# Performance work log

Hardware: AMD Instinct MI355X
Metric: run time of the kernel (lower is better)

The kernel has to match this reference:

```python
import jax, jax.numpy as jnp
import numpy as np
import math


def setup_inputs() -> dict:
    key = jax.random.key(0)
    n = 8192
    m = n * (n - 1) // 2  # 33550336
    compressed_matrix = jax.random.normal(key, (m,), dtype=jnp.float32)
    return {"compressed_matrix": compressed_matrix}


def reference(compressed_matrix) -> jnp.ndarray:
    m = compressed_matrix.shape[0]
    n = round(math.sqrt(2 * m)) + 1
    i, j = jnp.triu_indices(n, k=1)
    # scatter compressed vector into strict upper triangle
    upper = jnp.zeros((n, n), dtype=compressed_matrix.dtype).at[i, j].set(compressed_matrix)
    # symmetrize (diag of upper is zero, so subtracting diag is a no-op, kept for fidelity)
    sym = upper + upper.T - jnp.diag(jnp.diagonal(upper))
    return sym + jnp.eye(n, dtype=compressed_matrix.dtype)
```

## Files before the change

kernel.cpp:

```cpp
#include <hip/hip_runtime.h>
#include <math.h>

#define TILE 64

__global__ __launch_bounds__(256) void uncompress_sym_kernel(
    const float* __restrict__ comp, float* __restrict__ out, int n) {
    const int tr = blockIdx.y;
    const int tc = blockIdx.x;
    if (tc < tr) return;

    const int tid = threadIdx.x;
    __shared__ float s[TILE][TILE + 1];

    const int i0 = tr * TILE;
    const int j0 = tc * TILE;

    if (tr == tc) {
        for (int e = tid; e < TILE * TILE; e += 256) {
            const int y = e >> 6;
            const int x = e & 63;
            float v = 0.0f;
            if (x > y) {
                const int i = i0 + y;
                const int j = j0 + x;
                const int base = i * (2 * n - i - 1) / 2 - i - 1;
                v = comp[base + j];
            }
            s[y][x] = v;
        }
        __syncthreads();
        for (int e = tid; e < TILE * TILE; e += 256) {
            const int y = e >> 6;
            const int x = e & 63;
            float v;
            if (x > y)      v = s[y][x];
            else if (x == y) v = 1.0f;
            else            v = s[x][y];
            out[(size_t)(i0 + y) * n + (j0 + x)] = v;
        }
    } else {
        for (int it = 0; it < 4; ++it) {
            const int y  = (tid >> 4) + it * 16;
            const int x4 = (tid & 15) * 4;
            const int i  = i0 + y;
            const int base = i * (2 * n - i - 1) / 2 - i - 1;
            float4 v;
            __builtin_memcpy(&v, &comp[base + j0 + x4], sizeof(float4));
            *(float4*)&out[(size_t)i * n + (j0 + x4)] = v;
            s[y][x4 + 0] = v.x;
            s[y][x4 + 1] = v.y;
            s[y][x4 + 2] = v.z;
            s[y][x4 + 3] = v.w;
        }
        __syncthreads();
        for (int it = 0; it < 4; ++it) {
            const int y  = (tid >> 4) + it * 16;
            const int x4 = (tid & 15) * 4;
            float4 w;
            w.x = s[x4 + 0][y];
            w.y = s[x4 + 1][y];
            w.z = s[x4 + 2][y];
            w.w = s[x4 + 3][y];
            *(float4*)&out[(size_t)(j0 + y) * n + (i0 + x4)] = w;
        }
    }
}

extern "C" void kernel_launch(void* const* d_in, const int* in_sizes, int n_in,
                              void* d_out, int out_size, void* d_ws, size_t ws_size,
                              hipStream_t stream) {
    const float* comp = (const float*)d_in[0];
    float* out = (float*)d_out;
    const long long m = in_sizes[0];
    const int n = (int)llround(sqrt(2.0 * (double)m)) + 1;
    const int T = n / TILE;
    dim3 grid(T, T);
    uncompress_sym_kernel<<<grid, 256, 0, stream>>>(comp, out, n);
}
```

Before: 371.4 us.

## Launch only upper-triangle tiles, batch loads, use nontemporal stores

Replaces the full T×T grid, where half the blocks exit immediately, with a 1D grid over upper-triangle tiles only. Each block recovers its tile row and column from the linear block index with a sqrt estimate plus correction loops. All four row loads are issued before any store to expose more memory-level parallelism, and output writes use nontemporal stores so they do not pollute the cache. The cost is a few extra integer and float operations per block for the index mapping.

```diff
diff --git a/kernel.cpp b/kernel.cpp
--- a/kernel.cpp
+++ b/kernel.cpp
@@ -3,11 +3,16 @@
 
 #define TILE 64
 
+typedef float v4f  __attribute__((ext_vector_type(4)));
+typedef float v4fu __attribute__((ext_vector_type(4), aligned(4)));
+
 __global__ __launch_bounds__(256) void uncompress_sym_kernel(
-    const float* __restrict__ comp, float* __restrict__ out, int n) {
-    const int tr = blockIdx.y;
-    const int tc = blockIdx.x;
-    if (tc < tr) return;
+    const float* __restrict__ comp, float* __restrict__ out, int n, int T) {
+    const int b = blockIdx.x;
+    int tr = (int)((2 * T + 1 - sqrtf((float)((2 * T + 1) * (2 * T + 1) - 8 * b))) * 0.5f);
+    while (tr * T - tr * (tr - 1) / 2 > b) --tr;
+    while ((tr + 1) * T - (tr + 1) * tr / 2 <= b) ++tr;
+    const int tc = tr + (b - (tr * T - tr * (tr - 1) / 2));
 
     const int tid = threadIdx.x;
     __shared__ float s[TILE][TILE + 1];
@@ -15,16 +20,45 @@
     const int i0 = tr * TILE;
     const int j0 = tc * TILE;
 
-    if (tr == tc) {
+    if (tr != tc) {
+        const int x4 = (tid & 15) * 4;
+        const int yb = tid >> 4;
+        v4f v[4];
+#pragma unroll
+        for (int it = 0; it < 4; ++it) {
+            const int i = i0 + yb + it * 16;
+            const int base = i * (2 * n - i - 1) / 2 - i - 1;
+            v[it] = *(const v4fu*)&comp[base + j0 + x4];
+        }
+#pragma unroll
+        for (int it = 0; it < 4; ++it) {
+            const int y = yb + it * 16;
+            __builtin_nontemporal_store(v[it], (v4f*)&out[(size_t)(i0 + y) * n + (j0 + x4)]);
+            s[y][x4 + 0] = v[it].x;
+            s[y][x4 + 1] = v[it].y;
+            s[y][x4 + 2] = v[it].z;
+            s[y][x4 + 3] = v[it].w;
+        }
+        __syncthreads();
+#pragma unroll
+        for (int it = 0; it < 4; ++it) {
+            const int y = yb + it * 16;
+            v4f w;
+            w.x = s[x4 + 0][y];
+            w.y = s[x4 + 1][y];
+            w.z = s[x4 + 2][y];
+            w.w = s[x4 + 3][y];
+            __builtin_nontemporal_store(w, (v4f*)&out[(size_t)(j0 + y) * n + (i0 + x4)]);
+        }
+    } else {
         for (int e = tid; e < TILE * TILE; e += 256) {
             const int y = e >> 6;
             const int x = e & 63;
             float v = 0.0f;
             if (x > y) {
                 const int i = i0 + y;
-                const int j = j0 + x;
                 const int base = i * (2 * n - i - 1) / 2 - i - 1;
-                v = comp[base + j];
+                v = comp[base + j0 + x];
             }
             s[y][x] = v;
         }
@@ -33,35 +67,10 @@
             const int y = e >> 6;
             const int x = e & 63;
             float v;
-            if (x > y)      v = s[y][x];
+            if (x > y)       v = s[y][x];
             else if (x == y) v = 1.0f;
-            else            v = s[x][y];
-            out[(size_t)(i0 + y) * n + (j0 + x)] = v;
-        }
-    } else {
-        for (int it = 0; it < 4; ++it) {
-            const int y  = (tid >> 4) + it * 16;
-            const int x4 = (tid & 15) * 4;
-            const int i  = i0 + y;
-            const int base = i * (2 * n - i - 1) / 2 - i - 1;
-            float4 v;
-            __builtin_memcpy(&v, &comp[base + j0 + x4], sizeof(float4));
-            *(float4*)&out[(size_t)i * n + (j0 + x4)] = v;
-            s[y][x4 + 0] = v.x;
-            s[y][x4 + 1] = v.y;
-            s[y][x4 + 2] = v.z;
-            s[y][x4 + 3] = v.w;
-        }
-        __syncthreads();
-        for (int it = 0; it < 4; ++it) {
-            const int y  = (tid >> 4) + it * 16;
-            const int x4 = (tid & 15) * 4;
-            float4 w;
-            w.x = s[x4 + 0][y];
-            w.y = s[x4 + 1][y];
-            w.z = s[x4 + 2][y];
-            w.w = s[x4 + 3][y];
-            *(float4*)&out[(size_t)(j0 + y) * n + (i0 + x4)] = w;
+            else             v = s[x][y];
+            __builtin_nontemporal_store(v, &out[(size_t)(i0 + y) * n + (j0 + x)]);
         }
     }
 }
@@ -74,6 +83,6 @@
     const long long m = in_sizes[0];
     const int n = (int)llround(sqrt(2.0 * (double)m)) + 1;
     const int T = n / TILE;
-    dim3 grid(T, T);
-    uncompress_sym_kernel<<<grid, 256, 0, stream>>>(comp, out, n);
+    const int nblocks = T * (T + 1) / 2;
+    uncompress_sym_kernel<<<nblocks, 256, 0, stream>>>(comp, out, n, T);
 }
```

Result: no change. 372.7 us (+0.4%).
